# Performance work log

Hardware: AMD Instinct MI355X
Metric: run time of the kernel (lower is better)

## Reference

```python
import jax, jax.numpy as jnp
import numpy as np

N = 50000      # num nodes
E = 1_600_000  # num edges
D = 64         # in_dim == hidden_dim
H = 4          # heads
C = 16         # head_dim = hidden_dim // heads
NEG = 0.2      # leaky_relu negative slope (PyG GATConv default)


def setup_inputs() -> dict:
    key = jax.random.key(0)
    ks = jax.random.split(key, 20)
    f = lambda k, s: (jax.random.normal(k, s, jnp.float32) * 0.1)
    return dict(
        node_features=jax.random.normal(ks[0], (N, D), jnp.float32),
        edge_index=jax.random.randint(ks[1], (2, E), 0, N, dtype=jnp.int32),
        edge_type=jax.random.randint(ks[2], (E,), 0, 5, dtype=jnp.int32),
        edge_attr=jax.random.normal(ks[3], (E, 1), jnp.float32),
        # GAT layer 1 (PyG GATConv: lin has no bias, att_* are [H,C], final bias [H*C])
        W1=f(ks[4], (D, H * C)), att_src1=f(ks[5], (H, C)), att_dst1=f(ks[6], (H, C)),
        We1=f(ks[7], (1, H * C)), att_e1=f(ks[8], (H, C)), b1=jnp.zeros((H * C,), jnp.float32),
        # GAT layer 2
        W2=f(ks[9], (D, H * C)), att_src2=f(ks[10], (H, C)), att_dst2=f(ks[11], (H, C)),
        We2=f(ks[12], (1, H * C)), att_e2=f(ks[13], (H, C)), b2=jnp.zeros((H * C,), jnp.float32),
        # LayerNorms
        g1=jnp.ones((D,), jnp.float32), beta1=jnp.zeros((D,), jnp.float32),
        g2=jnp.ones((D,), jnp.float32), beta2=jnp.zeros((D,), jnp.float32),
        # output head
        Wout=f(ks[14], (D, 1)), bout=jnp.zeros((1,), jnp.float32),
    )


def _layernorm(x, g, b, eps=1e-5):
    mu = x.mean(-1, keepdims=True)
    v = ((x - mu) ** 2).mean(-1, keepdims=True)
    return (x - mu) * jax.lax.rsqrt(v + eps) * g + b


def _seg_softmax(alpha, dst, n):
    # numerically stable segment softmax over incoming edges of each dst node
    m = jax.ops.segment_max(alpha, dst, num_segments=n)
    m = jnp.where(jnp.isfinite(m), m, 0.0)
    ex = jnp.exp(alpha - m[dst])
    den = jax.ops.segment_sum(ex, dst, num_segments=n)
    return ex / (den[dst] + 1e-16)


def _gatconv(x, src, dst, eattr, W, a_s, a_d, We, a_e, b, n):
    xs = (x @ W).reshape(n, H, C)                       # [N,H,C]
    a_src = jnp.einsum('nhc,hc->nh', xs, a_s)           # [N,H]
    a_dst = jnp.einsum('nhc,hc->nh', xs, a_d)           # [N,H]
    ee = (eattr @ We).reshape(-1, H, C)                 # [E',H,C]
    a_edge = jnp.einsum('ehc,hc->eh', ee, a_e)          # [E',H]
    alpha = a_src[src] + a_dst[dst] + a_edge            # [E',H]
    alpha = jax.nn.leaky_relu(alpha, NEG)
    alpha = _seg_softmax(alpha, dst, n)                 # [E',H]
    msg = xs[src] * alpha[..., None]                    # [E',H,C] gather-weighted messages
    out = jax.ops.segment_sum(msg, dst, num_segments=n) # scatter-aggregate
    return out.reshape(n, H * C) + b


def reference(node_features, edge_index, edge_type, edge_attr,
              W1, att_src1, att_dst1, We1, att_e1, b1,
              W2, att_src2, att_dst2, We2, att_e2, b2,
              g1, beta1, g2, beta2, Wout, bout):
    src, dst = edge_index[0], edge_index[1]
    # PyG add_self_loops(fill_value='mean'): self-loop edge_attr = mean of edge_attr over incoming edges
    cnt = jax.ops.segment_sum(jnp.ones((E,), jnp.float32), dst, num_segments=N)
    loop_attr = jax.ops.segment_sum(edge_attr, dst, num_segments=N) / jnp.maximum(cnt, 1.0)[:, None]
    loops = jnp.arange(N, dtype=src.dtype)
    src2 = jnp.concatenate([src, loops])
    dst2 = jnp.concatenate([dst, loops])
    ea = jnp.concatenate([edge_attr, loop_attr], axis=0)

    residual = node_features  # in_dim == hidden_dim -> no res_proj
    h = _gatconv(node_features, src2, dst2, ea, W1, att_src1, att_dst1, We1, att_e1, b1, N)
    h = jax.nn.elu(_layernorm(h + residual, g1, beta1))
    residual = h
    h = _gatconv(h, src2, dst2, ea, W2, att_src2, att_dst2, We2, att_e2, b2, N)
    h = jax.nn.elu(_layernorm(h + residual, g2, beta2))
    return h @ Wout + bout
```

## Files before the change

### kernel.cpp

```cpp
#include <hip/hip_runtime.h>
#include <hip/hip_bf16.h>
#include <cfloat>

#define NN 50000
#define NE 1600000
#define NEG 0.2f
#define NBKT 196
#define BNODE 256
#define P1_TILE 2048
#define P1_BLOCKS 782
#define GEMM_BLOCKS 391
#define SCAP 40
#define SLOTS 96
#define L2E 1.4426950408889634f
#define SMEM_BYTES 10880

typedef __attribute__((ext_vector_type(8))) short bf8_t;
typedef __attribute__((ext_vector_type(4))) float f4_t;

__device__ __forceinline__ float bf16bits_to_f(unsigned v) {
  return __uint_as_float(v << 16);
}
__device__ __forceinline__ unsigned f_to_bf16bits(float f) {
  unsigned u = __float_as_uint(f);
  return (u + 0x7fffu + ((u >> 16) & 1u)) >> 16;
}

__device__ __forceinline__ bf8_t pack8(const float* p) {
  bf8_t r;
#pragma unroll
  for (int i = 0; i < 8; ++i) r[i] = (short)f_to_bf16bits(p[i]);
  return r;
}

__device__ void bin_body(char* smem, int blk, const int* __restrict__ src,
                         const int* __restrict__ dst,
                         const float* __restrict__ ea, int* __restrict__ scnt,
                         int2* __restrict__ gbuf) {
  int* lcur = (int*)smem;
  int t = threadIdx.x;
  if (t < NBKT) lcur[t] = 0;
  __syncthreads();
  int e0 = blk * P1_TILE + t * 8;
  int bb[8], vx[8], vy[8];
  if (e0 + 8 <= NE) {
    int4 d0 = *(const int4*)(dst + e0), d1 = *(const int4*)(dst + e0 + 4);
    int4 s0 = *(const int4*)(src + e0), s1 = *(const int4*)(src + e0 + 4);
    int4 a0 = *(const int4*)((const int*)ea + e0);
    int4 a1 = *(const int4*)((const int*)ea + e0 + 4);
    int dd[8] = {d0.x, d0.y, d0.z, d0.w, d1.x, d1.y, d1.z, d1.w};
    int ss[8] = {s0.x, s0.y, s0.z, s0.w, s1.x, s1.y, s1.z, s1.w};
    int aa[8] = {a0.x, a0.y, a0.z, a0.w, a1.x, a1.y, a1.z, a1.w};
#pragma unroll
    for (int k = 0; k < 8; ++k) {
      bb[k] = dd[k] >> 8;
      vx[k] = ((dd[k] & 255) << 16) | ss[k];
      vy[k] = aa[k];
    }
  } else {
#pragma unroll
    for (int k = 0; k < 8; ++k) {
      int e = e0 + k;
      if (e < NE) {
        int d = dst[e];
        bb[k] = d >> 8;
        vx[k] = ((d & 255) << 16) | src[e];
        vy[k] = __float_as_int(ea[e]);
      } else {
        bb[k] = -1;
      }
    }
  }
#pragma unroll
  for (int k = 0; k < 8; ++k) {
    if (bb[k] >= 0) {
      int pos = atomicAdd(&lcur[bb[k]], 1);
      if (pos < SCAP)
        gbuf[((size_t)bb[k] * P1_BLOCKS + blk) * SCAP + pos] =
            make_int2(vx[k], vy[k]);
    }
  }
  __syncthreads();
  if (t < NBKT) scnt[blk * NBKT + t] = min(lcur[t], SCAP);
}

template <bool FP32IN>
__device__ void gemm_body(char* smem, int blk, const void* __restrict__ xin,
                          const float* __restrict__ W,
                          const float* __restrict__ att_s,
                          const float* __restrict__ att_d,
                          unsigned short* __restrict__ xsb,
                          float* __restrict__ a_src,
                          float* __restrict__ a_dst) {
  unsigned short(*Wt)[68] = (unsigned short(*)[68])smem;
  int t = threadIdx.x;
  for (int i = t; i < 4096; i += 256) {
    int k = i >> 6, n = i & 63;
    Wt[n][k] = (unsigned short)f_to_bf16bits(W[i]);
  }
  __syncthreads();
  {
    int k = t & 63, h = t >> 6;
    float ps = 0.f, pd = 0.f;
#pragma unroll
    for (int c = 0; c < 16; ++c) {
      float w = bf16bits_to_f(Wt[h * 16 + c][k]);
      ps = fmaf(w, att_s[h * 16 + c], ps);
      pd = fmaf(w, att_d[h * 16 + c], pd);
    }
    Wt[64 + h][k] = (unsigned short)f_to_bf16bits(ps * L2E);
    Wt[68 + h][k] = (unsigned short)f_to_bf16bits(pd * L2E);
    Wt[72 + h][k] = 0;
    Wt[76 + h][k] = 0;
  }
  __syncthreads();
  int lane = t & 63, wave = t >> 6;
  int quad = lane >> 4, n16 = lane & 15;

  bf8_t bfrag[5][2];
#pragma unroll
  for (int nt = 0; nt < 5; ++nt)
#pragma unroll
    for (int kk = 0; kk < 2; ++kk)
      bfrag[nt][kk] = *(const bf8_t*)&Wt[nt * 16 + n16][kk * 32 + quad * 8];

#pragma unroll
  for (int set = 0; set < 2; ++set) {
    int r0 = blk * 128 + set * 64 + wave * 16;
    int rowA = r0 + n16; if (rowA > NN - 1) rowA = NN - 1;
    bf8_t af0, af1;
    if (FP32IN) {
      const float* xr = (const float*)xin + (size_t)rowA * 64 + quad * 8;
      af0 = pack8(xr);
      af1 = pack8(xr + 32);
    } else {
      const bf8_t* xrow =
          (const bf8_t*)((const unsigned short*)xin + (size_t)rowA * 64);
      af0 = xrow[quad];
      af1 = xrow[4 + quad];
    }
#pragma unroll
    for (int nt = 0; nt < 5; ++nt) {
      f4_t acc = {0.f, 0.f, 0.f, 0.f};
      acc = __builtin_amdgcn_mfma_f32_16x16x32_bf16(af0, bfrag[nt][0], acc, 0, 0, 0);
      acc = __builtin_amdgcn_mfma_f32_16x16x32_bf16(af1, bfrag[nt][1], acc, 0, 0, 0);
      if (nt < 4) {
#pragma unroll
        for (int reg = 0; reg < 4; ++reg) {
          int row = r0 + quad * 4 + reg;
          if (row < NN)
            xsb[(size_t)row * 64 + nt * 16 + n16] =
                (unsigned short)f_to_bf16bits(acc[reg]);
        }
      } else {
#pragma unroll
        for (int reg = 0; reg < 4; ++reg) {
          int row = r0 + quad * 4 + reg;
          if (row < NN && n16 < 8) {
            if (n16 < 4) a_src[row * 4 + n16] = acc[reg];
            else a_dst[row * 4 + (n16 - 4)] = acc[reg];
          }
        }
      }
    }
  }
}

__global__ __launch_bounds__(256) void front_kernel(
    const int* __restrict__ src, const int* __restrict__ dst,
    const float* __restrict__ ea, int* __restrict__ scnt,
    int2* __restrict__ gbuf, const float* __restrict__ x,
    const float* __restrict__ W1, const float* __restrict__ as1,
    const float* __restrict__ ad1, unsigned short* __restrict__ xsb,
    float* __restrict__ a_src, float* __restrict__ a_dst) {
  __shared__ __align__(16) char smem[SMEM_BYTES];
  if (blockIdx.x < P1_BLOCKS) {
    bin_body(smem, blockIdx.x, src, dst, ea, scnt, gbuf);
  } else {
    gemm_body<true>(smem, blockIdx.x - P1_BLOCKS, x, W1, as1, ad1, xsb, a_src,
                    a_dst);
  }
}

__global__ __launch_bounds__(256) void gemm2_kernel(
    const unsigned short* __restrict__ xin, const float* __restrict__ W,
    const float* __restrict__ att_s, const float* __restrict__ att_d,
    unsigned short* __restrict__ xsb, float* __restrict__ a_src,
    float* __restrict__ a_dst) {
  __shared__ __align__(16) char smem[SMEM_BYTES];
  gemm_body<false>(smem, blockIdx.x, xin, W, att_s, att_d, xsb, a_src, a_dst);
}

__global__ __launch_bounds__(1024) void build_kernel(
    const int* __restrict__ scnt, const int2* __restrict__ gbuf,
    int* __restrict__ cnt, unsigned* __restrict__ csr) {
  __shared__ int lc[BNODE];
  int t = threadIdx.x;
  int b = blockIdx.x;
  if (t < BNODE) lc[t] = 0;
  __syncthreads();
  for (int s = t; s < P1_BLOCKS; s += 1024) {
    int c = scnt[s * NBKT + b];
    const int2* p = gbuf + ((size_t)b * P1_BLOCKS + s) * SCAP;
    for (int i = 0; i < c; ++i) {
      int2 v = p[i];
      int dl = (v.x >> 16) & 255;
      int pos = atomicAdd(&lc[dl], 1);
      if (pos < SLOTS) {
        unsigned eb = ((unsigned)v.y) & 0xffff0000u;
        csr[(size_t)(b * BNODE + dl) * SLOTS + pos] =
            eb | (unsigned)(v.x & 0xffff);
      }
    }
  }
  __syncthreads();
  if (t < BNODE) {
    int n = b * BNODE + t;
    if (n < NN) cnt[n] = min(lc[t], SLOTS);
  }
}

template <bool HEAD>
__global__ __launch_bounds__(256) void aggregate_kernel(
    const int* __restrict__ cnt, const unsigned* __restrict__ csr,
    const unsigned short* __restrict__ xsb, const float* __restrict__ a_src,
    const float* __restrict__ a_dst, const float* __restrict__ We,
    const float* __restrict__ att_e, const float* __restrict__ bias,
    const void* __restrict__ resv, const float* __restrict__ g,
    const float* __restrict__ beta, const float* __restrict__ Wout,
    const float* __restrict__ bout, float* __restrict__ out,
    unsigned short* __restrict__ out_b) {
  __shared__ __align__(16) uint2 rec[4][64][4];
  int t = threadIdx.x;
  int lane = t & 63, wave = t >> 6;
  int half = lane >> 5;
  int d2 = lane & 31;
  int hb = d2 >> 3;
  int n = blockIdx.x * 8 + wave * 2 + half;

  float sp = We[lane] * att_e[lane];
#pragma unroll
  for (int off = 8; off; off >>= 1) sp += __shfl_xor(sp, off, 16);
  sp *= L2E;
  float s0 = __shfl(sp, 0, 64), s1 = __shfl(sp, 16, 64);
  float s2 = __shfl(sp, 32, 64), s3 = __shfl(sp, 48, 64);

  const float4 adv = *(const float4*)(a_dst + (size_t)n * 4);

  int dn = cnt[n];
  int mdn = max(dn, __shfl_xor(dn, 32, 64));
  float accx = 0.f, accy = 0.f, den = 0.f, easum = 0.f;
  const uint2* rpb = &rec[wave][half * 32][hb];
  const char* xd = (const char*)xsb + d2 * 4;

  for (int base = 0; base < mdn; base += 32) {
    int c = mdn - base; if (c > 32) c = 32;
    int el = base + d2;
    unsigned ce = (el < dn) ? csr[(size_t)n * SLOTS + el] : 0u;
    float ea = __uint_as_float(ce & 0xffff0000u);
    easum += ea;
    unsigned soff = (ce & 0xffffu) * 128u;
    float ex0 = 0.f, ex1 = 0.f, ex2 = 0.f, ex3 = 0.f;
    if (el < dn) {
      const float4 av = *(const float4*)(a_src + (size_t)(ce & 0xffffu) * 4);
      float a0 = av.x + fmaf(ea, s0, adv.x); a0 = fmaxf(a0, NEG * a0);
      float a1 = av.y + fmaf(ea, s1, adv.y); a1 = fmaxf(a1, NEG * a1);
      float a2 = av.z + fmaf(ea, s2, adv.z); a2 = fmaxf(a2, NEG * a2);
      float a3 = av.w + fmaf(ea, s3, adv.w); a3 = fmaxf(a3, NEG * a3);
      ex0 = exp2f(a0); ex1 = exp2f(a1); ex2 = exp2f(a2); ex3 = exp2f(a3);
    }
    uint4* wp = (uint4*)&rec[wave][lane][0];
    wp[0] = make_uint4(soff, __float_as_uint(ex0), soff, __float_as_uint(ex1));
    wp[1] = make_uint4(soff, __float_as_uint(ex2), soff, __float_as_uint(ex3));
    int c8 = (c + 7) & ~7;
    for (int j = 0; j < c8; j += 8) {
      uint2 v0 = rpb[(j + 0) * 4];
      uint2 v1 = rpb[(j + 1) * 4];
      uint2 v2 = rpb[(j + 2) * 4];
      uint2 v3 = rpb[(j + 3) * 4];
      uint2 v4 = rpb[(j + 4) * 4];
      uint2 v5 = rpb[(j + 5) * 4];
      uint2 v6 = rpb[(j + 6) * 4];
      uint2 v7 = rpb[(j + 7) * 4];
      unsigned u0 = *(const unsigned*)(xd + v0.x);
      unsigned u1 = *(const unsigned*)(xd + v1.x);
      unsigned u2 = *(const unsigned*)(xd + v2.x);
      unsigned u3 = *(const unsigned*)(xd + v3.x);
      unsigned u4 = *(const unsigned*)(xd + v4.x);
      unsigned u5 = *(const unsigned*)(xd + v5.x);
      unsigned u6 = *(const unsigned*)(xd + v6.x);
      unsigned u7 = *(const unsigned*)(xd + v7.x);
      float e0f = __uint_as_float(v0.y), e1f = __uint_as_float(v1.y);
      float e2f = __uint_as_float(v2.y), e3f = __uint_as_float(v3.y);
      float e4f = __uint_as_float(v4.y), e5f = __uint_as_float(v5.y);
      float e6f = __uint_as_float(v6.y), e7f = __uint_as_float(v7.y);
      den += ((e0f + e1f) + (e2f + e3f)) + ((e4f + e5f) + (e6f + e7f));
      accx = fmaf(e0f, __uint_as_float(u0 << 16), accx);
      accy = fmaf(e0f, __uint_as_float(u0 & 0xffff0000u), accy);
      accx = fmaf(e1f, __uint_as_float(u1 << 16), accx);
      accy = fmaf(e1f, __uint_as_float(u1 & 0xffff0000u), accy);
      accx = fmaf(e2f, __uint_as_float(u2 << 16), accx);
      accy = fmaf(e2f, __uint_as_float(u2 & 0xffff0000u), accy);
      accx = fmaf(e3f, __uint_as_float(u3 << 16), accx);
      accy = fmaf(e3f, __uint_as_float(u3 & 0xffff0000u), accy);
      accx = fmaf(e4f, __uint_as_float(u4 << 16), accx);
      accy = fmaf(e4f, __uint_as_float(u4 & 0xffff0000u), accy);
      accx = fmaf(e5f, __uint_as_float(u5 << 16), accx);
      accy = fmaf(e5f, __uint_as_float(u5 & 0xffff0000u), accy);
      accx = fmaf(e6f, __uint_as_float(u6 << 16), accx);
      accy = fmaf(e6f, __uint_as_float(u6 & 0xffff0000u), accy);
      accx = fmaf(e7f, __uint_as_float(u7 << 16), accx);
      accy = fmaf(e7f, __uint_as_float(u7 & 0xffff0000u), accy);
    }
  }

#pragma unroll
  for (int off = 16; off; off >>= 1) easum += __shfl_xor(easum, off, 32);

  float loop_ea = easum / fmaxf((float)dn, 1.0f);
  float as_h = a_src[(size_t)n * 4 + hb];
  float adn = (hb == 0) ? adv.x : (hb == 1) ? adv.y : (hb == 2) ? adv.z : adv.w;
  float sph = (hb == 0) ? s0 : (hb == 1) ? s1 : (hb == 2) ? s2 : s3;
  float a_self = as_h + fmaf(loop_ea, sph, adn);
  a_self = fmaxf(a_self, NEG * a_self);
  float ex_self = exp2f(a_self);
  den += ex_self;
  unsigned un = *(const unsigned*)((const char*)xsb + (size_t)n * 128 + d2 * 4);
  accx = fmaf(ex_self, __uint_as_float(un << 16), accx);
  accy = fmaf(ex_self, __uint_as_float(un & 0xffff0000u), accy);

  float rden = 1.f / (den + 1e-16f);
  const float2 bi = *(const float2*)(bias + d2 * 2);
  float2 rsd;
  if (HEAD) {
    unsigned ur =
        *(const unsigned*)((const unsigned short*)resv + (size_t)n * 64 + d2 * 2);
    rsd.x = bf16bits_to_f(ur & 0xffffu);
    rsd.y = __uint_as_float(ur & 0xffff0000u);
  } else {
    rsd = *(const float2*)((const float*)resv + (size_t)n * 64 + d2 * 2);
  }
  float vx = accx * rden + bi.x + rsd.x;
  float vy = accy * rden + bi.y + rsd.y;
  float s = vx + vy;
#pragma unroll
  for (int off = 16; off; off >>= 1) s += __shfl_xor(s, off, 32);
  float mu = s * (1.0f / 64.0f);
  float dx = vx - mu, dy = vy - mu;
  float var = dx * dx + dy * dy;
#pragma unroll
  for (int off = 16; off; off >>= 1) var += __shfl_xor(var, off, 32);
  var *= (1.0f / 64.0f);
  float rstd = rsqrtf(var + 1e-5f);
  const float2 gg = *(const float2*)(g + d2 * 2);
  const float2 bb = *(const float2*)(beta + d2 * 2);
  float yx = dx * rstd * gg.x + bb.x;
  float yy = dy * rstd * gg.y + bb.y;
  yx = yx > 0.f ? yx : expm1f(yx);
  yy = yy > 0.f ? yy : expm1f(yy);
  if (HEAD) {
    const float2 wv = *(const float2*)(Wout + d2 * 2);
    float p = yx * wv.x + yy * wv.y;
#pragma unroll
    for (int off = 16; off; off >>= 1) p += __shfl_xor(p, off, 32);
    if (d2 == 0) out[n] = p + bout[0];
  } else {
    unsigned ob = f_to_bf16bits(yx) | (f_to_bf16bits(yy) << 16);
    *(unsigned*)(out_b + (size_t)n * 64 + d2 * 2) = ob;
  }
}

extern "C" void kernel_launch(void* const* d_in, const int* in_sizes, int n_in,
                              void* d_out, int out_size, void* d_ws,
                              size_t ws_size, hipStream_t stream) {
  const float* node_features = (const float*)d_in[0];
  const int* edge_index = (const int*)d_in[1];
  const int* src = edge_index;
  const int* dst = edge_index + NE;
  const float* edge_attr = (const float*)d_in[3];
  const float* W1 = (const float*)d_in[4];
  const float* att_src1 = (const float*)d_in[5];
  const float* att_dst1 = (const float*)d_in[6];
  const float* We1 = (const float*)d_in[7];
  const float* att_e1 = (const float*)d_in[8];
  const float* b1 = (const float*)d_in[9];
  const float* W2 = (const float*)d_in[10];
  const float* att_src2 = (const float*)d_in[11];
  const float* att_dst2 = (const float*)d_in[12];
  const float* We2 = (const float*)d_in[13];
  const float* att_e2 = (const float*)d_in[14];
  const float* b2 = (const float*)d_in[15];
  const float* g1 = (const float*)d_in[16];
  const float* beta1 = (const float*)d_in[17];
  const float* g2 = (const float*)d_in[18];
  const float* beta2 = (const float*)d_in[19];
  const float* Wout = (const float*)d_in[20];
  const float* bout = (const float*)d_in[21];
  float* out = (float*)d_out;

  char* ws = (char*)d_ws;
  size_t o = 0;
  auto alloc = [&](size_t bytes) {
    void* p = ws + o;
    o += (bytes + 255) & ~(size_t)255;
    return p;
  };
  int* scnt = (int*)alloc((size_t)P1_BLOCKS * NBKT * 4);
  int2* gbuf = (int2*)alloc((size_t)NBKT * P1_BLOCKS * SCAP * 8);
  int* cnt = (int*)alloc((size_t)NN * 4);
  unsigned* csr = (unsigned*)alloc((size_t)NN * SLOTS * 4);
  unsigned short* xsb = (unsigned short*)alloc((size_t)NN * 64 * 2);
  unsigned short* h1b = (unsigned short*)alloc((size_t)NN * 64 * 2);
  float* a_srcb = (float*)alloc((size_t)NN * 4 * 4);
  float* a_dstb = (float*)alloc((size_t)NN * 4 * 4);

  front_kernel<<<P1_BLOCKS + GEMM_BLOCKS, 256, 0, stream>>>(
      src, dst, edge_attr, scnt, gbuf, node_features, W1, att_src1, att_dst1,
      xsb, a_srcb, a_dstb);
  build_kernel<<<NBKT, 1024, 0, stream>>>(scnt, gbuf, cnt, csr);

  aggregate_kernel<false><<<NN / 8, 256, 0, stream>>>(
      cnt, csr, xsb, a_srcb, a_dstb, We1, att_e1, b1, node_features, g1, beta1,
      nullptr, nullptr, nullptr, h1b);

  gemm2_kernel<<<GEMM_BLOCKS, 256, 0, stream>>>(h1b, W2, att_src2, att_dst2,
                                                xsb, a_srcb, a_dstb);
  aggregate_kernel<true><<<NN / 8, 256, 0, stream>>>(
      cnt, csr, xsb, a_srcb, a_dstb, We2, att_e2, b2, h1b, g2, beta2, Wout,
      bout, out, nullptr);
}
```

Measured before the change: 235.2 us.

## Fuse layer-2 projection GEMM into layer-1 aggregate epilogue

Removes the separate gemm2 kernel launch. The layer-1 aggregate kernel now computes each node's layer-2 projection (h1 @ W2) right after LayerNorm/ELU, using a bf16-packed W2 staged in LDS, together with the attention src/dst logits. W2 is pre-packed to bf16 pairs by block 0 of build_kernel. This saves a launch and a reread of h1 from global memory, but the projection moves from MFMA to scalar FMAs, and every aggregate block pays an LDS fill of W2 plus an extra barrier.

```diff
diff --git a/kernel.cpp b/kernel.cpp
--- a/kernel.cpp
+++ b/kernel.cpp
@@ -84,8 +84,7 @@
   if (t < NBKT) scnt[blk * NBKT + t] = min(lcur[t], SCAP);
 }
 
-template <bool FP32IN>
-__device__ void gemm_body(char* smem, int blk, const void* __restrict__ xin,
+__device__ void gemm_body(char* smem, int blk, const float* __restrict__ xin,
                           const float* __restrict__ W,
                           const float* __restrict__ att_s,
                           const float* __restrict__ att_d,
@@ -128,17 +127,9 @@
   for (int set = 0; set < 2; ++set) {
     int r0 = blk * 128 + set * 64 + wave * 16;
     int rowA = r0 + n16; if (rowA > NN - 1) rowA = NN - 1;
-    bf8_t af0, af1;
-    if (FP32IN) {
-      const float* xr = (const float*)xin + (size_t)rowA * 64 + quad * 8;
-      af0 = pack8(xr);
-      af1 = pack8(xr + 32);
-    } else {
-      const bf8_t* xrow =
-          (const bf8_t*)((const unsigned short*)xin + (size_t)rowA * 64);
-      af0 = xrow[quad];
-      af1 = xrow[4 + quad];
-    }
+    const float* xr = xin + (size_t)rowA * 64 + quad * 8;
+    bf8_t af0 = pack8(xr);
+    bf8_t af1 = pack8(xr + 32);
 #pragma unroll
     for (int nt = 0; nt < 5; ++nt) {
       f4_t acc = {0.f, 0.f, 0.f, 0.f};
@@ -177,26 +168,26 @@
   if (blockIdx.x < P1_BLOCKS) {
     bin_body(smem, blockIdx.x, src, dst, ea, scnt, gbuf);
   } else {
-    gemm_body<true>(smem, blockIdx.x - P1_BLOCKS, x, W1, as1, ad1, xsb, a_src,
-                    a_dst);
-  }
-}
-
-__global__ __launch_bounds__(256) void gemm2_kernel(
-    const unsigned short* __restrict__ xin, const float* __restrict__ W,
-    const float* __restrict__ att_s, const float* __restrict__ att_d,
-    unsigned short* __restrict__ xsb, float* __restrict__ a_src,
-    float* __restrict__ a_dst) {
-  __shared__ __align__(16) char smem[SMEM_BYTES];
-  gemm_body<false>(smem, blockIdx.x, xin, W, att_s, att_d, xsb, a_src, a_dst);
+    gemm_body(smem, blockIdx.x - P1_BLOCKS, x, W1, as1, ad1, xsb, a_src,
+              a_dst);
+  }
 }
 
 __global__ __launch_bounds__(1024) void build_kernel(
     const int* __restrict__ scnt, const int2* __restrict__ gbuf,
-    int* __restrict__ cnt, unsigned* __restrict__ csr) {
+    int* __restrict__ cnt, unsigned* __restrict__ csr,
+    const float* __restrict__ W2, unsigned* __restrict__ w2p) {
   __shared__ int lc[BNODE];
   int t = threadIdx.x;
   int b = blockIdx.x;
+  if (b == 0) {
+    for (int i = t; i < 2048; i += 1024) {
+      int j = i >> 5, m = i & 31;
+      unsigned lo = f_to_bf16bits(W2[(2 * m) * 64 + j]);
+      unsigned hi = f_to_bf16bits(W2[(2 * m + 1) * 64 + j]);
+      w2p[i] = lo | (hi << 16);
+    }
+  }
   if (t < BNODE) lc[t] = 0;
   __syncthreads();
   for (int s = t; s < P1_BLOCKS; s += 1024) {
@@ -229,9 +220,27 @@
     const void* __restrict__ resv, const float* __restrict__ g,
     const float* __restrict__ beta, const float* __restrict__ Wout,
     const float* __restrict__ bout, float* __restrict__ out,
-    unsigned short* __restrict__ out_b) {
+    unsigned short* __restrict__ out_b, const unsigned* __restrict__ w2p,
+    const float* __restrict__ as2v, const float* __restrict__ ad2v,
+    unsigned short* __restrict__ xsb2, float* __restrict__ a_src2,
+    float* __restrict__ a_dst2) {
   __shared__ __align__(16) uint2 rec[4][64][4];
+  __shared__ unsigned W2L[64 * 33];
+  __shared__ __align__(16) unsigned h1row[4][2][32];
   int t = threadIdx.x;
+  if (!HEAD) {
+    const uint4* wp4 = (const uint4*)w2p;
+#pragma unroll
+    for (int r = 0; r < 2; ++r) {
+      int i4 = t + r * 256;
+      uint4 v = wp4[i4];
+      int idx = i4 * 4;
+      int j = idx >> 5, m = idx & 31;
+      unsigned* wl = &W2L[j * 33 + m];
+      wl[0] = v.x; wl[1] = v.y; wl[2] = v.z; wl[3] = v.w;
+    }
+    __syncthreads();
+  }
   int lane = t & 63, wave = t >> 6;
   int half = lane >> 5;
   int d2 = lane & 31;
@@ -364,9 +373,47 @@
 #pragma unroll
     for (int off = 16; off; off >>= 1) p += __shfl_xor(p, off, 32);
     if (d2 == 0) out[n] = p + bout[0];
-  } else {
-    unsigned ob = f_to_bf16bits(yx) | (f_to_bf16bits(yy) << 16);
-    *(unsigned*)(out_b + (size_t)n * 64 + d2 * 2) = ob;
+    return;
+  }
+  unsigned hpair = f_to_bf16bits(yx) | (f_to_bf16bits(yy) << 16);
+  *(unsigned*)(out_b + (size_t)n * 64 + d2 * 2) = hpair;
+  h1row[wave][half][d2] = hpair;
+
+#pragma unroll 1
+  for (int p = 0; p < 2; ++p) {
+    int np = blockIdx.x * 8 + wave * 2 + p;
+    const uint4* hp4 = (const uint4*)&h1row[wave][p][0];
+    const unsigned* wc = &W2L[lane * 33];
+    float acc2 = 0.f;
+#pragma unroll
+    for (int m8 = 0; m8 < 8; ++m8) {
+      uint4 h4 = hp4[m8];
+      unsigned w0 = wc[m8 * 4 + 0], w1 = wc[m8 * 4 + 1];
+      unsigned w2b = wc[m8 * 4 + 2], w3 = wc[m8 * 4 + 3];
+      acc2 = fmaf(__uint_as_float(h4.x << 16), __uint_as_float(w0 << 16), acc2);
+      acc2 = fmaf(__uint_as_float(h4.x & 0xffff0000u),
+                  __uint_as_float(w0 & 0xffff0000u), acc2);
+      acc2 = fmaf(__uint_as_float(h4.y << 16), __uint_as_float(w1 << 16), acc2);
+      acc2 = fmaf(__uint_as_float(h4.y & 0xffff0000u),
+                  __uint_as_float(w1 & 0xffff0000u), acc2);
+      acc2 = fmaf(__uint_as_float(h4.z << 16), __uint_as_float(w2b << 16), acc2);
+      acc2 = fmaf(__uint_as_float(h4.z & 0xffff0000u),
+                  __uint_as_float(w2b & 0xffff0000u), acc2);
+      acc2 = fmaf(__uint_as_float(h4.w << 16), __uint_as_float(w3 << 16), acc2);
+      acc2 = fmaf(__uint_as_float(h4.w & 0xffff0000u),
+                  __uint_as_float(w3 & 0xffff0000u), acc2);
+    }
+    xsb2[(size_t)np * 64 + lane] = (unsigned short)f_to_bf16bits(acc2);
+    float ps = acc2 * as2v[lane], pd = acc2 * ad2v[lane];
+#pragma unroll
+    for (int off = 8; off; off >>= 1) {
+      ps += __shfl_xor(ps, off, 16);
+      pd += __shfl_xor(pd, off, 16);
+    }
+    if ((lane & 15) == 0) {
+      a_src2[(size_t)np * 4 + (lane >> 4)] = ps * L2E;
+      a_dst2[(size_t)np * 4 + (lane >> 4)] = pd * L2E;
+    }
   }
 }
 
@@ -410,22 +457,26 @@
   int* cnt = (int*)alloc((size_t)NN * 4);
   unsigned* csr = (unsigned*)alloc((size_t)NN * SLOTS * 4);
   unsigned short* xsb = (unsigned short*)alloc((size_t)NN * 64 * 2);
+  unsigned short* xsb2 = (unsigned short*)alloc((size_t)NN * 64 * 2);
   unsigned short* h1b = (unsigned short*)alloc((size_t)NN * 64 * 2);
   float* a_srcb = (float*)alloc((size_t)NN * 4 * 4);
   float* a_dstb = (float*)alloc((size_t)NN * 4 * 4);
+  float* a_src2 = (float*)alloc((size_t)NN * 4 * 4);
+  float* a_dst2 = (float*)alloc((size_t)NN * 4 * 4);
+  unsigned* w2p = (unsigned*)alloc(2048 * 4);
 
   front_kernel<<<P1_BLOCKS + GEMM_BLOCKS, 256, 0, stream>>>(
       src, dst, edge_attr, scnt, gbuf, node_features, W1, att_src1, att_dst1,
       xsb, a_srcb, a_dstb);
-  build_kernel<<<NBKT, 1024, 0, stream>>>(scnt, gbuf, cnt, csr);
+  build_kernel<<<NBKT, 1024, 0, stream>>>(scnt, gbuf, cnt, csr, W2, w2p);
 
   aggregate_kernel<false><<<NN / 8, 256, 0, stream>>>(
       cnt, csr, xsb, a_srcb, a_dstb, We1, att_e1, b1, node_features, g1, beta1,
-      nullptr, nullptr, nullptr, h1b);
-
-  gemm2_kernel<<<GEMM_BLOCKS, 256, 0, stream>>>(h1b, W2, att_src2, att_dst2,
-                                                xsb, a_srcb, a_dstb);
+      nullptr, nullptr, nullptr, h1b, w2p, att_src2, att_dst2, xsb2, a_src2,
+      a_dst2);
+
   aggregate_kernel<true><<<NN / 8, 256, 0, stream>>>(
-      cnt, csr, xsb, a_srcb, a_dstb, We2, att_e2, b2, h1b, g2, beta2, Wout,
-      bout, out, nullptr);
-}
+      cnt, csr, xsb2, a_src2, a_dst2, We2, att_e2, b2, h1b, g2, beta2, Wout,
+      bout, out, nullptr, nullptr, nullptr, nullptr, nullptr, nullptr,
+      nullptr);
+}
```

Result: no change. 233.6 us (-0.7%).
